# Kernel tuning notes

Hardware: AMD Instinct MI355X
Metric: run time of the kernel (lower is better)

The kernel has to match this reference:

```python
import jax, jax.numpy as jnp
import numpy as np

B, S, D, H = 2, 2048, 2048, 16
HD = D // H  # 128
ROPE_BASE = 10000.0


def _rope_tables(seq_len, head_dim, dtype=jnp.float32):
    inv_freq = 1.0 / (ROPE_BASE ** (jnp.arange(0, head_dim, 2, dtype=jnp.float32) / head_dim))
    t = jnp.arange(seq_len, dtype=jnp.float32)
    freqs = jnp.outer(t, inv_freq)  # [S, HD/2]
    # broadcast shape [1, S, 1, HD/2]
    return jnp.cos(freqs)[None, :, None, :].astype(dtype), jnp.sin(freqs)[None, :, None, :].astype(dtype)


def _apply_rope(x, cos, sin):
    # x: [B, S, H, HD]; interleaved split, output concatenated by halves (matches torch code)
    x1 = x[..., ::2]
    x2 = x[..., 1::2]
    return jnp.concatenate([x1 * cos - x2 * sin, x1 * sin + x2 * cos], axis=-1)


def setup_inputs() -> dict:
    key = jax.random.key(0)
    ks = jax.random.split(key, 9)
    xavier = lambda k: jax.random.uniform(k, (D, D), jnp.float32, -1.0, 1.0) * np.sqrt(6.0 / (D + D))
    return {
        "x": jax.random.normal(ks[0], (B, S, D), jnp.float32),
        "attention_mask": jnp.ones((B, S), jnp.int32),
        "wq": xavier(ks[1]), "bq": jnp.zeros((D,), jnp.float32),
        "wk": xavier(ks[2]), "bk": jnp.zeros((D,), jnp.float32),
        "wv": xavier(ks[3]), "bv": jnp.zeros((D,), jnp.float32),
        "wo": xavier(ks[4]), "bo": jnp.zeros((D,), jnp.float32),
    }


def reference(x, attention_mask, wq, bq, wk, bk, wv, bv, wo, bo):
    b, s, _ = x.shape
    scale = HD ** -0.5
    q = (x @ wq + bq).reshape(b, s, H, HD)
    k = (x @ wk + bk).reshape(b, s, H, HD)
    v = (x @ wv + bv).reshape(b, s, H, HD)
    cos, sin = _rope_tables(s, HD, x.dtype)
    q = _apply_rope(q, cos, sin)
    k = _apply_rope(k, cos, sin)
    # [B, H, S, S]
    scores = jnp.einsum('bqhd,bkhd->bhqk', q, k) * scale
    mask = attention_mask[:, None, None, :]  # 2D mask -> [B,1,1,S]
    scores = jnp.where(mask == 0, jnp.asarray(-1e9, scores.dtype), scores)
    attn = jax.nn.softmax(scores, axis=-1)
    out = jnp.einsum('bhqk,bkhd->bqhd', attn, v).reshape(b, s, D)
    return out @ wo + bo
```

## Files before the change

kernel.cpp:

```cpp
#include <hip/hip_runtime.h>

#define Bc 2
#define Sc 2048
#define Dc 2048
#define Hc 16
#define HDc 128
#define Mc 4096

typedef __bf16 bf16_t;
typedef __bf16 bf16x4 __attribute__((ext_vector_type(4)));
typedef __bf16 bf16x8 __attribute__((ext_vector_type(8)));
typedef float f32x4 __attribute__((ext_vector_type(4)));
typedef float f32x16 __attribute__((ext_vector_type(16)));

__device__ __forceinline__ f32x4 mfma16(bf16x8 a, bf16x8 b, f32x4 c) {
  return __builtin_amdgcn_mfma_f32_16x16x32_bf16(a, b, c, 0, 0, 0);
}
__device__ __forceinline__ f32x16 mfma32(bf16x8 a, bf16x8 b, f32x16 c) {
  return __builtin_amdgcn_mfma_f32_32x32x16_bf16(a, b, c, 0, 0, 0);
}

typedef const unsigned __attribute__((address_space(1))) gu32_t;
typedef unsigned __attribute__((address_space(3))) lu32_t;

__device__ __forceinline__ void gload_lds16(const void* g, void* l) {
  gu32_t* gp = (gu32_t*)(unsigned long long)g;
  lu32_t* lp = (lu32_t*)(unsigned)(unsigned long long)l;
  __builtin_amdgcn_global_load_lds(gp, lp, 16, 0, 0);
}

__device__ __forceinline__ unsigned cvtpk(float lo, float hi_) {
  unsigned r;
  asm("v_cvt_pk_bf16_f32 %0, %1, %2" : "=v"(r) : "v"(lo), "v"(hi_));
  return r;
}
__device__ __forceinline__ void plswap(unsigned& a, unsigned& b) {
  asm volatile("v_permlane32_swap_b32 %0, %1" : "+v"(a), "+v"(b));
}

__global__ void cvt_bf16_kernel(const float* __restrict__ in, bf16_t* __restrict__ out, int n4) {
  int i = blockIdx.x * blockDim.x + threadIdx.x;
  if (i < n4) {
    float4 v = ((const float4*)in)[i];
    bf16x4 o;
    o[0] = (bf16_t)v.x; o[1] = (bf16_t)v.y; o[2] = (bf16_t)v.z; o[3] = (bf16_t)v.w;
    ((bf16x4*)out)[i] = o;
  }
}

__global__ void transpose_cvt_kernel(const float* __restrict__ w, bf16_t* __restrict__ wt) {
  __shared__ float tile[32][33];
  const int tx = threadIdx.x, ty = threadIdx.y;
  const int n0 = blockIdx.x * 32, k0 = blockIdx.y * 32;
#pragma unroll
  for (int i = 0; i < 32; i += 8)
    tile[ty + i][tx] = w[(size_t)(k0 + ty + i) * Dc + n0 + tx];
  __syncthreads();
#pragma unroll
  for (int i = 0; i < 32; i += 8)
    wt[(size_t)(n0 + ty + i) * Dc + k0 + tx] = (bf16_t)tile[tx][ty + i];
}

template <int MODE, int NT>
__global__ __launch_bounds__(512, 1) void gemmx_kernel(
    const bf16_t* __restrict__ A, const bf16_t* __restrict__ Bt,
    const float* __restrict__ bias0, const float* __restrict__ bias1,
    const float* __restrict__ bias2,
    void* __restrict__ out0, void* __restrict__ out1, void* __restrict__ out2) {
  __shared__ __align__(16) bf16_t sA[3][256 * 32];
  __shared__ __align__(16) bf16_t sB[3][256 * 32];
  const int tid = threadIdx.x;
  const int lane = tid & 63, wid = tid >> 6;
  const int l15 = lane & 15, g = lane >> 4;
  const int wrow = wid >> 2, wcol = wid & 3;

  const int nwg = 16 * NT, cpx = nwg / 8;
  const int wgid = ((int)blockIdx.x & 7) * cpx + ((int)blockIdx.x >> 3);
  const int nt = wgid % NT, mt = wgid / NT;
  const int m0 = mt * 256, n0 = nt * 256;

  const bf16_t* Ab = A + (size_t)m0 * 2048;
  const bf16_t* Bb = Bt + (size_t)n0 * 2048;

#define GX_STAGE(kt)                                                  \
  {                                                                   \
    const int sl_ = (kt) % 3;                                         \
    _Pragma("unroll") for (int i_ = 0; i_ < 2; ++i_) {                \
      int s_ = i_ * 512 + tid;                                        \
      int rp_ = s_ >> 3, cs_ = (s_ & 7) ^ (rp_ & 7);                  \
      int sr_ = 2 * rp_ + (cs_ >> 2);                                 \
      int sk_ = (kt) * 32 + (cs_ & 3) * 8;                            \
      gload_lds16(Ab + (size_t)sr_ * 2048 + sk_,                      \
                  (char*)&sA[sl_][0] + s_ * 16);                      \
    }                                                                 \
    _Pragma("unroll") for (int i_ = 0; i_ < 2; ++i_) {                \
      int s_ = i_ * 512 + tid;                                        \
      int rp_ = s_ >> 3, cs_ = (s_ & 7) ^ (rp_ & 7);                  \
      int sr_ = 2 * rp_ + (cs_ >> 2);                                 \
      int sk_ = (kt) * 32 + (cs_ & 3) * 8;                            \
      gload_lds16(Bb + (size_t)sr_ * 2048 + sk_,                      \
                  (char*)&sB[sl_][0] + s_ * 16);                      \
    }                                                                 \
  }

  f32x4 acc[8][4] = {};

  GX_STAGE(0);
  GX_STAGE(1);

#define GX_BODY(t, DOSTG, VMSTR)                                             \
  {                                                                          \
    asm volatile("s_waitcnt vmcnt(" VMSTR ")" ::: "memory");                 \
    __builtin_amdgcn_s_barrier(); \
    __builtin_amdgcn_sched_barrier(0);                                       \
    const char* pA = (const char*)&sA[(t) % 3][0];                           \
    const char* pB = (const char*)&sB[(t) % 3][0];                           \
    bf16x8 af[8], bfr[4];                                                    \
    _Pragma("unroll") for (int mi = 0; mi < 8; ++mi) {                       \
      int ra = wrow * 128 + mi * 16 + l15;                                   \
      int rp = ra >> 1, cs = (ra & 1) * 4 + g;                               \
      af[mi] = *(const bf16x8*)(pA + rp * 128 + ((cs ^ (rp & 7)) * 16));     \
    }                                                                        \
    _Pragma("unroll") for (int ni = 0; ni < 4; ++ni) {                       \
      int rb = wcol * 64 + ni * 16 + l15;                                    \
      int rp = rb >> 1, cs = (rb & 1) * 4 + g;                               \
      bfr[ni] = *(const bf16x8*)(pB + rp * 128 + ((cs ^ (rp & 7)) * 16));    \
    }                                                                        \
    if (DOSTG) GX_STAGE((t) + 2);                                            \
    __builtin_amdgcn_s_setprio(1);                                           \
    _Pragma("unroll") for (int mi = 0; mi < 8; ++mi)                         \
      _Pragma("unroll") for (int ni = 0; ni < 4; ++ni)                       \
          acc[mi][ni] = mfma16(af[mi], bfr[ni], acc[mi][ni]);                \
    __builtin_amdgcn_s_setprio(0);                                           \
  }

  for (int t = 0; t < 62; ++t) GX_BODY(t, 1, "4");
  GX_BODY(62, 0, "4");
  GX_BODY(63, 0, "0");

#undef GX_BODY
#undef GX_STAGE

#pragma unroll
  for (int mi = 0; mi < 8; ++mi) {
#pragma unroll
    for (int ni = 0; ni < 4; ++ni) {
      const int ncol = n0 + wcol * 64 + ni * 16 + l15;
      if (MODE == 2) {
        const float bv = bias0[ncol];
#pragma unroll
        for (int r = 0; r < 4; ++r) {
          const int mrow = m0 + wrow * 128 + mi * 16 + g * 4 + r;
          ((float*)out0)[(size_t)mrow * 2048 + ncol] = acc[mi][ni][r] + bv;
        }
      } else {
        const int proj = ncol >> 11, nloc = ncol & 2047;
        const float* bp = proj == 0 ? bias0 : (proj == 1 ? bias1 : bias2);
        bf16_t* op = (bf16_t*)(proj == 0 ? out0 : (proj == 1 ? out1 : out2));
        const float bv = bp[nloc];
        const int h = nloc >> 7, hd = nloc & 127;
#pragma unroll
        for (int r = 0; r < 4; ++r) {
          const int mrow = m0 + wrow * 128 + mi * 16 + g * 4 + r;
          const int b = mrow >> 11, sq = mrow & 2047;
          const float v = acc[mi][ni][r] + bv;
          if (proj < 2)
            op[(((size_t)(b * Hc + h) * Sc + sq) * HDc) + hd] = (bf16_t)v;
          else
            op[(((size_t)(b * Hc + h) * HDc + hd) * Sc) + sq] = (bf16_t)v;
        }
      }
    }
  }
}

__global__ __launch_bounds__(256) void rope_kernel(bf16_t* __restrict__ qk) {
  const int w = threadIdx.x >> 6, lane = threadIdx.x & 63;
  const long row = (long)blockIdx.x * 4 + w;
  const int s = (int)(row & (Sc - 1));
  bf16_t* p = qk + row * HDc;
  float x1 = (float)p[2 * lane];
  float x2 = (float)p[2 * lane + 1];
  float freq = expf(-(float)lane * (9.210340371976184f / 64.0f));
  float ang = (float)s * freq;
  float sn, cs;
  sincosf(ang, &sn, &cs);
  __syncthreads();
  p[lane] = (bf16_t)(x1 * cs - x2 * sn);
  p[lane + 64] = (bf16_t)(x1 * sn + x2 * cs);
}

__global__ __launch_bounds__(256, 2) void attn_kernel(
    const bf16_t* __restrict__ Q, const bf16_t* __restrict__ Kr,
    const bf16_t* __restrict__ Vt, const int* __restrict__ mask,
    bf16_t* __restrict__ AO) {
  __shared__ __align__(16) bf16_t sK[2][64 * 128];
  __shared__ __align__(16) bf16_t sV[2][64 * 128];
  __shared__ float mbias[Sc];
  __shared__ float bcast[4][32];
  const int tid = threadIdx.x;
  const int w = tid >> 6, lane = tid & 63;
  const int l31 = lane & 31, hi = lane >> 5;
  const int wbase = w * 64;

  const int bid = blockIdx.x;
  const int L = ((bid & 7) << 6) + (bid >> 3);
  const int qc = L & 15, h = (L >> 4) & 15, b = L >> 8;

  const int* mb = mask + b * Sc;
#pragma unroll
  for (int i = 0; i < Sc / 256; ++i)
    mbias[i * 256 + tid] = mb[i * 256 + tid] ? 0.f : -1e9f;

  const int q0 = qc * 128 + w * 32;
  const bf16_t* qb = Q + ((size_t)(b * Hc + h) * Sc + q0) * HDc;
  const bf16_t* kb = Kr + ((size_t)(b * Hc + h) * Sc) * HDc;
  const bf16_t* vb = Vt + ((size_t)(b * Hc + h) * HDc) * Sc;

  bf16x8 qf[8];
  {
    const bf16_t* qr = qb + (size_t)l31 * HDc + hi * 8;
#pragma unroll
    for (int kk = 0; kk < 8; ++kk) qf[kk] = *(const bf16x8*)(qr + kk * 16);
  }

#define STAGE_KV(sKb, sVb, kv0_)                                             \
  {                                                                          \
    _Pragma("unroll") for (int p = 0; p < 4; ++p) {                          \
      int s_ = p * 256 + tid;                                                \
      int rk = s_ >> 4, ck = s_ & 15;                                        \
      gload_lds16(kb + (size_t)((kv0_) + rk) * HDc + ((ck ^ (rk & 15)) * 8), \
                  (char*)(sKb) + (size_t)(p * 256 + wbase) * 16);            \
      int d63 = s_ >> 4, sv = s_ & 15;                                       \
      int tmp = sv ^ (d63 & 15);                                             \
      int hb = tmp >> 3, cv = tmp & 7;                                       \
      gload_lds16(vb + (size_t)(hb * 64 + d63) * Sc + (kv0_) + cv * 8,       \
                  (char*)(sVb) + (size_t)(p * 256 + wbase) * 16);            \
    }                                                                        \
  }

  bf16_t* sKc = &sK[0][0];
  bf16_t* sKn = &sK[1][0];
  bf16_t* sVc = &sV[0][0];
  bf16_t* sVn = &sV[1][0];

  STAGE_KV(sKc, sVc, 0);
  asm volatile("s_waitcnt vmcnt(0)" ::: "memory");
  __syncthreads();

  f32x16 acc[4];
#pragma unroll
  for (int d = 0; d < 4; ++d) acc[d] = 0.f;
  float mrun = -3.0e38f, lrun = 0.f;
  const float scale = 0.08838834764831845f;

  for (int kv0 = 0; kv0 < Sc; kv0 += 64) {
    if (kv0 + 64 < Sc) STAGE_KV(sKn, sVn, kv0 + 64);

    f32x16 s0 = 0.f, s1 = 0.f;
    {
      const char* kbase = (const char*)sKc;
      __builtin_amdgcn_s_setprio(1);
#pragma unroll
      for (int kk = 0; kk < 8; ++kk) {
        bf16x8 k0f = *(const bf16x8*)(kbase + l31 * 256 + (((2 * kk + hi) ^ (l31 & 15)) * 16));
        bf16x8 k1f = *(const bf16x8*)(kbase + (32 + l31) * 256 + (((2 * kk + hi) ^ ((32 + l31) & 15)) * 16));
        s0 = mfma32(k0f, qf[kk], s0);
        s1 = mfma32(k1f, qf[kk], s1);
      }
      __builtin_amdgcn_s_setprio(0);
    }
    float v[32];
    {
      const float* mp = mbias + kv0 + 4 * hi;
#pragma unroll
      for (int g4 = 0; g4 < 4; ++g4) {
        f32x4 b0 = *(const f32x4*)(mp + 8 * g4);
        f32x4 b1 = *(const f32x4*)(mp + 32 + 8 * g4);
#pragma unroll
        for (int j = 0; j < 4; ++j) {
          v[g4 * 4 + j] = s0[g4 * 4 + j] * scale + b0[j];
          v[16 + g4 * 4 + j] = s1[g4 * 4 + j] * scale + b1[j];
        }
      }
    }
    float tm = v[0];
#pragma unroll
    for (int r = 1; r < 32; ++r) tm = fmaxf(tm, v[r]);
    tm = fmaxf(tm, __shfl_xor(tm, 32));
    if (__any(tm > mrun + 8.f)) {
      float mnew = fmaxf(mrun, tm);
      float al = __expf(mrun - mnew);
      mrun = mnew;
      lrun *= al;
      bcast[w][l31] = al;
      asm volatile("s_waitcnt lgkmcnt(0)" ::: "memory");
      __builtin_amdgcn_sched_barrier(0);
#pragma unroll
      for (int g4 = 0; g4 < 4; ++g4) {
        f32x4 alr = *(const f32x4*)(&bcast[w][8 * g4 + 4 * hi]);
#pragma unroll
        for (int dblk = 0; dblk < 4; ++dblk)
#pragma unroll
          for (int j = 0; j < 4; ++j) acc[dblk][g4 * 4 + j] *= alr[j];
      }
    }
    float ts = 0.f;
#pragma unroll
    for (int r = 0; r < 32; ++r) {
      v[r] = __expf(v[r] - mrun);
      ts += v[r];
    }
    ts += __shfl_xor(ts, 32);
    lrun += ts;
    unsigned pk[4][4];
#pragma unroll
    for (int ks = 0; ks < 4; ++ks) {
      unsigned a1 = cvtpk(v[ks * 8 + 0], v[ks * 8 + 1]);
      unsigned b1 = cvtpk(v[ks * 8 + 4], v[ks * 8 + 5]);
      unsigned a2 = cvtpk(v[ks * 8 + 2], v[ks * 8 + 3]);
      unsigned b2 = cvtpk(v[ks * 8 + 6], v[ks * 8 + 7]);
      plswap(a1, b1);
      plswap(a2, b2);
      pk[ks][0] = a1; pk[ks][1] = a2; pk[ks][2] = b1; pk[ks][3] = b2;
    }
    {
      const char* vbase = (const char*)sVc;
      __builtin_amdgcn_s_setprio(1);
#pragma unroll
      for (int ks = 0; ks < 4; ++ks) {
        bf16x8 pa = *(const bf16x8*)&pk[ks][0];
#pragma unroll
        for (int dblk = 0; dblk < 4; ++dblk) {
          int d = dblk * 32 + l31;
          int slot = (((d >> 6) * 8 + (2 * ks + hi)) ^ (d & 15));
          bf16x8 vf = *(const bf16x8*)(vbase + (d & 63) * 256 + slot * 16);
          acc[dblk] = mfma32(pa, vf, acc[dblk]);
        }
      }
      __builtin_amdgcn_s_setprio(0);
    }
    asm volatile("s_waitcnt vmcnt(0)" ::: "memory");
    __syncthreads();
    bf16_t* t1 = sKc; sKc = sKn; sKn = t1;
    bf16_t* t2 = sVc; sVc = sVn; sVn = t2;
  }

  float inv = 1.f / lrun;
  bcast[w][l31] = inv;
  asm volatile("s_waitcnt lgkmcnt(0)" ::: "memory");
  __builtin_amdgcn_sched_barrier(0);
  bf16_t* ob = AO + ((size_t)b * Sc + q0) * Dc + h * HDc;
#pragma unroll
  for (int g4 = 0; g4 < 4; ++g4) {
    f32x4 ir = *(const f32x4*)(&bcast[w][8 * g4 + 4 * hi]);
#pragma unroll
    for (int j = 0; j < 4; ++j) {
      int q = 8 * g4 + 4 * hi + j;
#pragma unroll
      for (int dblk = 0; dblk < 4; ++dblk)
        ob[(size_t)q * Dc + dblk * 32 + l31] = (bf16_t)(acc[dblk][g4 * 4 + j] * ir[j]);
    }
  }
}

#define MB(x) ((size_t)(x) << 20)

extern "C" void kernel_launch(void* const* d_in, const int* in_sizes, int n_in,
                              void* d_out, int out_size, void* d_ws, size_t ws_size,
                              hipStream_t stream) {
  const float* x = (const float*)d_in[0];
  const int* mask = (const int*)d_in[1];
  const float* wq = (const float*)d_in[2];
  const float* bq = (const float*)d_in[3];
  const float* wk = (const float*)d_in[4];
  const float* bk = (const float*)d_in[5];
  const float* wv = (const float*)d_in[6];
  const float* bv = (const float*)d_in[7];
  const float* wo = (const float*)d_in[8];
  const float* bo = (const float*)d_in[9];
  float* out = (float*)d_out;

  char* ws = (char*)d_ws;
  bf16_t* xb     = (bf16_t*)(ws + MB(0));
  bf16_t* wqkvT  = (bf16_t*)(ws + MB(16));
  bf16_t* woT    = (bf16_t*)(ws + MB(40));
  bf16_t* qbuf   = (bf16_t*)(ws + MB(48));
  bf16_t* kbuf   = (bf16_t*)(ws + MB(64));
  bf16_t* vtb    = (bf16_t*)(ws + MB(80));
  bf16_t* ao     = (bf16_t*)(ws + MB(96));

  cvt_bf16_kernel<<<8192, 256, 0, stream>>>(x, xb, (Mc * Dc) / 4);

  dim3 tg(64, 64), tb(32, 8);
  transpose_cvt_kernel<<<tg, tb, 0, stream>>>(wq, wqkvT);
  transpose_cvt_kernel<<<tg, tb, 0, stream>>>(wk, wqkvT + (size_t)Dc * Dc);
  transpose_cvt_kernel<<<tg, tb, 0, stream>>>(wv, wqkvT + 2 * (size_t)Dc * Dc);
  transpose_cvt_kernel<<<tg, tb, 0, stream>>>(wo, woT);

  gemmx_kernel<0, 24><<<384, 512, 0, stream>>>(xb, wqkvT, bq, bk, bv, qbuf, kbuf, vtb);

  rope_kernel<<<(2 * Bc * Hc * Sc) / 4, 256, 0, stream>>>(qbuf);

  attn_kernel<<<Bc * Hc * (Sc / 128), 256, 0, stream>>>(qbuf, kbuf, vtb, mask, ao);

  gemmx_kernel<2, 8><<<128, 512, 0, stream>>>(ao, woT, bo, bo, bo, out, out, out);
}
```

Measured before the change: 326.8 us.

## Replace 256x256 GEMM tiles with 128x128 tiles, 4 waves, double buffering

Both projection GEMMs move from 256x256 tiles with 8 waves and a triple-buffered LDS pipeline to 128x128 tiles with 4 waves, two LDS buffers and launch bounds allowing several blocks per CU. The aim is better CU fill: 1536 and 512 blocks instead of 384 and 128 on the device's CUs, with the latency hiding coming from multiple resident blocks rather than deep prefetch. The cost is lower arithmetic intensity per tile, more global and L2 traffic, and a full vmcnt(0) wait plus barrier every K step.

```diff
diff --git a/kernel.cpp b/kernel.cpp
--- a/kernel.cpp
+++ b/kernel.cpp
@@ -62,31 +62,31 @@
 }
 
 template <int MODE, int NT>
-__global__ __launch_bounds__(512, 1) void gemmx_kernel(
+__global__ __launch_bounds__(256, 4) void gemmf_kernel(
     const bf16_t* __restrict__ A, const bf16_t* __restrict__ Bt,
     const float* __restrict__ bias0, const float* __restrict__ bias1,
     const float* __restrict__ bias2,
     void* __restrict__ out0, void* __restrict__ out1, void* __restrict__ out2) {
-  __shared__ __align__(16) bf16_t sA[3][256 * 32];
-  __shared__ __align__(16) bf16_t sB[3][256 * 32];
+  __shared__ __align__(16) bf16_t sA[2][64 * 64];
+  __shared__ __align__(16) bf16_t sB[2][64 * 64];
   const int tid = threadIdx.x;
   const int lane = tid & 63, wid = tid >> 6;
   const int l15 = lane & 15, g = lane >> 4;
-  const int wrow = wid >> 2, wcol = wid & 3;
-
-  const int nwg = 16 * NT, cpx = nwg / 8;
+  const int wr = wid >> 1, wc = wid & 1;
+
+  const int nwg = 32 * NT, cpx = nwg / 8;
   const int wgid = ((int)blockIdx.x & 7) * cpx + ((int)blockIdx.x >> 3);
   const int nt = wgid % NT, mt = wgid / NT;
-  const int m0 = mt * 256, n0 = nt * 256;
+  const int m0 = mt * 128, n0 = nt * 128;
 
   const bf16_t* Ab = A + (size_t)m0 * 2048;
   const bf16_t* Bb = Bt + (size_t)n0 * 2048;
 
-#define GX_STAGE(kt)                                                  \
+#define GF_STAGE(kt)                                                  \
   {                                                                   \
-    const int sl_ = (kt) % 3;                                         \
+    const int sl_ = (kt) & 1;                                         \
     _Pragma("unroll") for (int i_ = 0; i_ < 2; ++i_) {                \
-      int s_ = i_ * 512 + tid;                                        \
+      int s_ = i_ * 256 + tid;                                        \
       int rp_ = s_ >> 3, cs_ = (s_ & 7) ^ (rp_ & 7);                  \
       int sr_ = 2 * rp_ + (cs_ >> 2);                                 \
       int sk_ = (kt) * 32 + (cs_ & 3) * 8;                            \
@@ -94,7 +94,7 @@
                   (char*)&sA[sl_][0] + s_ * 16);                      \
     }                                                                 \
     _Pragma("unroll") for (int i_ = 0; i_ < 2; ++i_) {                \
-      int s_ = i_ * 512 + tid;                                        \
+      int s_ = i_ * 256 + tid;                                        \
       int rp_ = s_ >> 3, cs_ = (s_ & 7) ^ (rp_ & 7);                  \
       int sr_ = 2 * rp_ + (cs_ >> 2);                                 \
       int sk_ = (kt) * 32 + (cs_ & 3) * 8;                            \
@@ -103,54 +103,55 @@
     }                                                                 \
   }
 
-  f32x4 acc[8][4] = {};
-
-  GX_STAGE(0);
-  GX_STAGE(1);
-
-#define GX_BODY(t, DOSTG, VMSTR)                                             \
-  {                                                                          \
-    asm volatile("s_waitcnt vmcnt(" VMSTR ")" ::: "memory");                 \
-    __builtin_amdgcn_s_barrier(); \
-    __builtin_amdgcn_sched_barrier(0);                                       \
-    const char* pA = (const char*)&sA[(t) % 3][0];                           \
-    const char* pB = (const char*)&sB[(t) % 3][0];                           \
-    bf16x8 af[8], bfr[4];                                                    \
-    _Pragma("unroll") for (int mi = 0; mi < 8; ++mi) {                       \
-      int ra = wrow * 128 + mi * 16 + l15;                                   \
-      int rp = ra >> 1, cs = (ra & 1) * 4 + g;                               \
-      af[mi] = *(const bf16x8*)(pA + rp * 128 + ((cs ^ (rp & 7)) * 16));     \
-    }                                                                        \
-    _Pragma("unroll") for (int ni = 0; ni < 4; ++ni) {                       \
-      int rb = wcol * 64 + ni * 16 + l15;                                    \
-      int rp = rb >> 1, cs = (rb & 1) * 4 + g;                               \
-      bfr[ni] = *(const bf16x8*)(pB + rp * 128 + ((cs ^ (rp & 7)) * 16));    \
-    }                                                                        \
-    if (DOSTG) GX_STAGE((t) + 2);                                            \
-    __builtin_amdgcn_s_setprio(1);                                           \
-    _Pragma("unroll") for (int mi = 0; mi < 8; ++mi)                         \
-      _Pragma("unroll") for (int ni = 0; ni < 4; ++ni)                       \
-          acc[mi][ni] = mfma16(af[mi], bfr[ni], acc[mi][ni]);                \
-    __builtin_amdgcn_s_setprio(0);                                           \
-  }
-
-  for (int t = 0; t < 62; ++t) GX_BODY(t, 1, "4");
-  GX_BODY(62, 0, "4");
-  GX_BODY(63, 0, "0");
-
-#undef GX_BODY
-#undef GX_STAGE
-
-#pragma unroll
-  for (int mi = 0; mi < 8; ++mi) {
+  f32x4 acc[4][4] = {};
+
+  GF_STAGE(0);
+  asm volatile("s_waitcnt vmcnt(0)" ::: "memory");
+  __builtin_amdgcn_s_barrier();
+  __builtin_amdgcn_sched_barrier(0);
+
+#pragma unroll 2
+  for (int t = 0; t < 64; ++t) {
+    if (t < 63) GF_STAGE(t + 1);
+    const char* pA = (const char*)&sA[t & 1][0];
+    const char* pB = (const char*)&sB[t & 1][0];
+    bf16x8 af[4], bfr[4];
+#pragma unroll
+    for (int mi = 0; mi < 4; ++mi) {
+      int ra = wr * 64 + mi * 16 + l15;
+      int rp = ra >> 1, cs = (ra & 1) * 4 + g;
+      af[mi] = *(const bf16x8*)(pA + rp * 128 + ((cs ^ (rp & 7)) * 16));
+    }
 #pragma unroll
     for (int ni = 0; ni < 4; ++ni) {
-      const int ncol = n0 + wcol * 64 + ni * 16 + l15;
+      int rb = wc * 64 + ni * 16 + l15;
+      int rp = rb >> 1, cs = (rb & 1) * 4 + g;
+      bfr[ni] = *(const bf16x8*)(pB + rp * 128 + ((cs ^ (rp & 7)) * 16));
+    }
+    __builtin_amdgcn_s_setprio(1);
+#pragma unroll
+    for (int mi = 0; mi < 4; ++mi)
+#pragma unroll
+      for (int ni = 0; ni < 4; ++ni)
+        acc[mi][ni] = mfma16(af[mi], bfr[ni], acc[mi][ni]);
+    __builtin_amdgcn_s_setprio(0);
+    asm volatile("s_waitcnt vmcnt(0)" ::: "memory");
+    __builtin_amdgcn_s_barrier();
+    __builtin_amdgcn_sched_barrier(0);
+  }
+
+#undef GF_STAGE
+
+#pragma unroll
+  for (int mi = 0; mi < 4; ++mi) {
+#pragma unroll
+    for (int ni = 0; ni < 4; ++ni) {
+      const int ncol = n0 + wc * 64 + ni * 16 + l15;
       if (MODE == 2) {
         const float bv = bias0[ncol];
 #pragma unroll
         for (int r = 0; r < 4; ++r) {
-          const int mrow = m0 + wrow * 128 + mi * 16 + g * 4 + r;
+          const int mrow = m0 + wr * 64 + mi * 16 + g * 4 + r;
           ((float*)out0)[(size_t)mrow * 2048 + ncol] = acc[mi][ni][r] + bv;
         }
       } else {
@@ -161,7 +162,7 @@
         const int h = nloc >> 7, hd = nloc & 127;
 #pragma unroll
         for (int r = 0; r < 4; ++r) {
-          const int mrow = m0 + wrow * 128 + mi * 16 + g * 4 + r;
+          const int mrow = m0 + wr * 64 + mi * 16 + g * 4 + r;
           const int b = mrow >> 11, sq = mrow & 2047;
           const float v = acc[mi][ni][r] + bv;
           if (proj < 2)
@@ -398,11 +399,11 @@
   transpose_cvt_kernel<<<tg, tb, 0, stream>>>(wv, wqkvT + 2 * (size_t)Dc * Dc);
   transpose_cvt_kernel<<<tg, tb, 0, stream>>>(wo, woT);
 
-  gemmx_kernel<0, 24><<<384, 512, 0, stream>>>(xb, wqkvT, bq, bk, bv, qbuf, kbuf, vtb);
+  gemmf_kernel<0, 48><<<1536, 256, 0, stream>>>(xb, wqkvT, bq, bk, bv, qbuf, kbuf, vtb);
 
   rope_kernel<<<(2 * Bc * Hc * Sc) / 4, 256, 0, stream>>>(qbuf);
 
   attn_kernel<<<Bc * Hc * (Sc / 128), 256, 0, stream>>>(qbuf, kbuf, vtb, mask, ao);
 
-  gemmx_kernel<2, 8><<<128, 512, 0, stream>>>(ao, woT, bo, bo, bo, out, out, out);
-}
+  gemmf_kernel<2, 16><<<512, 256, 0, stream>>>(ao, woT, bo, bo, bo, out, out, out);
+}
```

Result: no change. 326.3 us (-0.1%).
